# Optimization experiments

Measured on AMD Instinct MI355X. Metric: run time of the kernel, lower is better.

Reference implementation:

```python
import jax, jax.numpy as jnp
import numpy as np

DIM = 96; NH = 3; HD = DIM // NH; SCALE = HD ** -0.5
WS = (7, 7, 7); N = WS[0] * WS[1] * WS[2]
SHIFT = (3, 3, 3)  # half window
NL = 2
GRID = (28, 28, 28)
B = 2


def _rel_index():
    wd, wh, ww = WS
    coords = np.stack(np.meshgrid(np.arange(wd), np.arange(wh), np.arange(ww), indexing='ij')).reshape(3, -1)
    rel = (coords[:, :, None] - coords[:, None, :]).transpose(1, 2, 0)  # [N,N,3]
    rel[..., 0] += wd - 1; rel[..., 1] += wh - 1; rel[..., 2] += ww - 1
    rel[..., 0] *= (2 * wh - 1) * (2 * ww - 1); rel[..., 1] *= (2 * ww - 1)
    return rel.sum(-1)  # [N,N]

REL_IDX = _rel_index()


def _window_partition(x):
    b, D, H, W, C = x.shape
    wd, wh, ww = WS
    x = x.reshape(b, D // wd, wd, H // wh, wh, W // ww, ww, C)
    x = x.transpose(0, 1, 3, 5, 2, 4, 6, 7)
    return x.reshape(-1, N, C)


def _window_reverse(win, b, D, H, W):
    wd, wh, ww = WS
    C = win.shape[-1]
    x = win.reshape(b, D // wd, H // wh, W // ww, wd, wh, ww, C)
    x = x.transpose(0, 1, 4, 2, 5, 3, 6, 7)
    return x.reshape(b, D, H, W, C)


def _compute_mask():
    # MONAI compute_mask for the shifted (SW-MSA) block
    D, H, W = GRID; wd, wh, ww = WS; sd, sh, sw = SHIFT
    img = np.zeros((1, D, H, W, 1), np.float32)
    cnt = 0
    for d in (slice(-wd), slice(-wd, -sd), slice(-sd, None)):
        for h in (slice(-wh), slice(-wh, -sh), slice(-sh, None)):
            for w in (slice(-ww), slice(-ww, -sw), slice(-sw, None)):
                img[:, d, h, w, :] = cnt; cnt += 1
    mw = img.reshape(1, D // wd, wd, H // wh, wh, W // ww, ww, 1)
    mw = mw.transpose(0, 1, 3, 5, 2, 4, 6, 7).reshape(-1, N)  # [nw, N]
    am = mw[:, None, :] - mw[:, :, None]
    return np.where(am != 0, np.float32(-100.0), np.float32(0.0))

MASK = jnp.asarray(_compute_mask())  # [nw, N, N]


def _ln(x, g, b):
    mu = x.mean(-1, keepdims=True)
    var = ((x - mu) ** 2).mean(-1, keepdims=True)
    return (x - mu) / jnp.sqrt(var + 1e-5) * g + b


def _block(x, p, shift, mask):
    b, D, H, W, C = x.shape
    h = _ln(x, p['n1g'], p['n1b'])
    if shift is not None:
        h = jnp.roll(h, (-shift[0], -shift[1], -shift[2]), axis=(1, 2, 3))
    xw = _window_partition(h)  # [b*nw, N, C]
    Bn = xw.shape[0]
    qkv = (xw @ p['qkvw'].T + p['qkvb']).reshape(Bn, N, 3, NH, HD).transpose(2, 0, 3, 1, 4)
    q, k, v = qkv[0] * SCALE, qkv[1], qkv[2]
    attn = jnp.einsum('bhnd,bhmd->bhnm', q, k)
    bias = p['rel'][REL_IDX.reshape(-1)].reshape(N, N, NH).transpose(2, 0, 1)
    attn = attn + bias[None]
    if mask is not None:
        nw = mask.shape[0]
        attn = (attn.reshape(Bn // nw, nw, NH, N, N) + mask[None, :, None]).reshape(Bn, NH, N, N)
    attn = jax.nn.softmax(attn, axis=-1)
    out = jnp.einsum('bhnm,bhmd->bhnd', attn, v).transpose(0, 2, 1, 3).reshape(Bn, N, C)
    out = out @ p['projw'].T + p['projb']
    h = _window_reverse(out, b, D, H, W)
    if shift is not None:
        h = jnp.roll(h, shift, axis=(1, 2, 3))
    x = x + h
    m = _ln(x, p['n2g'], p['n2b'])
    m = jax.nn.gelu(m @ p['fc1w'].T + p['fc1b'], approximate=False) @ p['fc2w'].T + p['fc2b']
    return x + m


def setup_inputs() -> dict:
    key = jax.random.key(0)
    ks = jax.random.split(key, 8)
    nbias = (2 * WS[0] - 1) * (2 * WS[1] - 1) * (2 * WS[2] - 1)
    return {
        'x': jax.random.normal(ks[0], (B,) + GRID + (DIM,), jnp.float32),
        'norm1_g': jnp.ones((NL, DIM), jnp.float32),
        'norm1_b': jnp.zeros((NL, DIM), jnp.float32),
        'qkv_w': jax.random.normal(ks[1], (NL, 3 * DIM, DIM), jnp.float32) * 0.02,
        'qkv_b': jnp.zeros((NL, 3 * DIM), jnp.float32),
        'rel_bias': jax.random.normal(ks[2], (NL, nbias, NH), jnp.float32) * 0.02,
        'proj_w': jax.random.normal(ks[3], (NL, DIM, DIM), jnp.float32) * 0.02,
        'proj_b': jnp.zeros((NL, DIM), jnp.float32),
        'norm2_g': jnp.ones((NL, DIM), jnp.float32),
        'norm2_b': jnp.zeros((NL, DIM), jnp.float32),
        'fc1_w': jax.random.normal(ks[4], (NL, 4 * DIM, DIM), jnp.float32) * 0.02,
        'fc1_b': jnp.zeros((NL, 4 * DIM), jnp.float32),
        'fc2_w': jax.random.normal(ks[5], (NL, DIM, 4 * DIM), jnp.float32) * 0.02,
        'fc2_b': jnp.zeros((NL, DIM), jnp.float32),
    }


def reference(x, norm1_g, norm1_b, qkv_w, qkv_b, rel_bias, proj_w, proj_b,
              norm2_g, norm2_b, fc1_w, fc1_b, fc2_w, fc2_b):
    for i in range(NL):
        p = dict(n1g=norm1_g[i], n1b=norm1_b[i], qkvw=qkv_w[i], qkvb=qkv_b[i],
                 rel=rel_bias[i], projw=proj_w[i], projb=proj_b[i],
                 n2g=norm2_g[i], n2b=norm2_b[i], fc1w=fc1_w[i], fc1b=fc1_b[i],
                 fc2w=fc2_w[i], fc2b=fc2_b[i])
        if i % 2 == 0:
            x = _block(x, p, None, None)  # W-MSA (mask is all-zero for shift=0)
        else:
            x = _block(x, p, SHIFT, MASK)  # SW-MSA
    return x
```

## Files before the change

kernel.cpp:

```cpp
#include <hip/hip_runtime.h>
#include <math.h>

#define DIM 96
#define NHD 3
#define HD 32
#define NWT 343
#define NWIN 128
#define TOK 43904
#define NBIAS 2197
#define SCALE 0.17677669529663687f
#define TPAD 352
#define QTS 5632
#define HSZ (22 * QTS)

typedef __attribute__((ext_vector_type(8))) short bf16x8;
typedef __attribute__((ext_vector_type(4))) float f32x4;

__device__ __forceinline__ unsigned short f2b(float f) {
    union { float f; unsigned int u; } x; x.f = f;
    unsigned int r = (x.u + 0x7fffu + ((x.u >> 16) & 1u)) >> 16;
    return (unsigned short)r;
}
__device__ __forceinline__ unsigned int pk2bf(float a, float b) {
    union { float f; unsigned int u; } x, y; x.f = a; y.f = b;
    return ((x.u + 0x8000u) >> 16) | ((y.u + 0x8000u) & 0xffff0000u);
}
__device__ __forceinline__ float lo16(unsigned int u) {
    union { unsigned int u; float f; } x; x.u = u << 16; return x.f;
}
__device__ __forceinline__ float hi16(unsigned int u) {
    union { unsigned int u; float f; } x; x.u = u & 0xffff0000u; return x.f;
}

__global__ void __launch_bounds__(256) k_cvt4(
        const float* __restrict__ s0, const float* __restrict__ s1,
        const float* __restrict__ s2, const float* __restrict__ s3,
        unsigned short* __restrict__ dst) {
    int i = blockIdx.x * 256 + threadIdx.x;
    if (i >= 221184) return;
    const float* src; int off;
    if (i < 55296)       { src = s0; off = i; }
    else if (i < 73728)  { src = s1; off = i - 55296; }
    else if (i < 147456) { src = s2; off = i - 73728; }
    else                 { src = s3; off = i - 147456; }
    dst[i] = f2b(src[off]);
}

__global__ void __launch_bounds__(256) k_bias(
        const float* __restrict__ rel0, const float* __restrict__ rel1,
        unsigned short* __restrict__ bt) {
    int i = blockIdx.x * 256 + threadIdx.x;
    if (i >= 27 * HSZ) return;
    int off = i % QTS;
    int t = i / QTS;
    int qt = t % 22; t /= 22;
    int head = t % 3; int combo = t / 3;
    int j = off & 7, q4i = (off >> 3) & 3, lm = (off >> 5) & 15, pr = off >> 9;
    int q = min(qt * 16 + lm, 342);
    int kcol = pr * 32 + ((j >> 2) << 4) + q4i * 4 + (j & 3);
    float outv;
    if (kcol >= 343) {
        outv = -100000.0f;
    } else {
        int dq = q / 49, hq = (q / 7) % 7, wq = q % 7;
        int dk = kcol / 49, hk = (kcol / 7) % 7, wk = kcol % 7;
        int ridx = (dq - dk + 6) * 169 + (hq - hk + 6) * 13 + (wq - wk + 6);
        const float* rel = (combo == 0) ? rel0 : rel1;
        float b = rel[ridx * 3 + head];
        if (combo > 0) {
            int ty = combo - 1;
            int rqd = (ty & 4) ? 1 + (dq >= 4) : 0;
            int rqh = (ty & 2) ? 1 + (hq >= 4) : 0;
            int rqw = (ty & 1) ? 1 + (wq >= 4) : 0;
            int rkd = (ty & 4) ? 1 + (dk >= 4) : 0;
            int rkh = (ty & 2) ? 1 + (hk >= 4) : 0;
            int rkw = (ty & 1) ? 1 + (wk >= 4) : 0;
            if (rqd != rkd || rqh != rkh || rqw != rkw) b -= 100.0f;
        }
        outv = b;
    }
    bt[i] = f2b(outv);
}

__global__ void __launch_bounds__(256) k_qkv(
        const float* __restrict__ x, const float* __restrict__ g1,
        const float* __restrict__ b1, const unsigned short* __restrict__ W,
        const float* __restrict__ bias, unsigned short* __restrict__ q,
        unsigned short* __restrict__ k, unsigned short* __restrict__ v, int shift) {
    __shared__ __align__(16) unsigned short lns[64][104];
    __shared__ __align__(16) unsigned short wbuf[96][104];
    int wid = threadIdx.x >> 6, lane = threadIdx.x & 63;
    int lm = lane & 15, q4 = lane >> 4;
    int m0 = blockIdx.x * 64 + wid * 16;
    int bwr[4], nnr[4];
    size_t rowoff[4];
    #pragma unroll
    for (int r = 0; r < 4; ++r) {
        int wtok = m0 + q4 * 4 + r;
        int bw = wtok / NWT, n = wtok % NWT;
        bwr[r] = bw; nnr[r] = n;
        int b = bw >> 6, win = bw & 63;
        int wdi = win >> 4, whi = (win >> 2) & 3, wwi = win & 3;
        int d = n / 49, h = (n / 7) % 7, w = n % 7;
        int sd = (wdi * 7 + d + shift) % 28;
        int sh = (whi * 7 + h + shift) % 28;
        int sw = (wwi * 7 + w + shift) % 28;
        rowoff[r] = (((size_t)(b * 28 + sd) * 28 + sh) * 28 + sw) * 96;
    }
    float val[6][4], g1v[6], b1v[6];
    #pragma unroll
    for (int c = 0; c < 6; ++c) {
        int ncol = c * 16 + lm;
        g1v[c] = g1[ncol]; b1v[c] = b1[ncol];
        #pragma unroll
        for (int r = 0; r < 4; ++r) val[c][r] = x[rowoff[r] + ncol];
    }
    #pragma unroll
    for (int r = 0; r < 4; ++r) {
        float s = 0.f, s2 = 0.f;
        #pragma unroll
        for (int c = 0; c < 6; ++c) { s += val[c][r]; s2 += val[c][r] * val[c][r]; }
        #pragma unroll
        for (int off = 8; off > 0; off >>= 1) {
            s  += __shfl_xor(s,  off, 64);
            s2 += __shfl_xor(s2, off, 64);
        }
        float mu = s * (1.0f / 96.0f);
        float rstd = rsqrtf(s2 * (1.0f / 96.0f) - mu * mu + 1e-5f);
        int row = wid * 16 + q4 * 4 + r;
        #pragma unroll
        for (int c = 0; c < 6; ++c)
            lns[row][c * 16 + lm] = f2b((val[c][r] - mu) * rstd * g1v[c] + b1v[c]);
    }
    __syncthreads();
    bf16x8 a1[3];
    #pragma unroll
    for (int ks = 0; ks < 3; ++ks)
        a1[ks] = *((const bf16x8*)&lns[wid * 16 + lm][ks * 32 + q4 * 8]);
    for (int ch = 0; ch < 3; ++ch) {
        __syncthreads();
        const uint4* src = (const uint4*)(W + ch * 96 * 96);
        for (int s = threadIdx.x; s < 1152; s += 256) {
            int row = s / 12, seg = s % 12;
            *((uint4*)&wbuf[row][seg * 8]) = src[s];
        }
        __syncthreads();
        f32x4 acc[6];
        #pragma unroll
        for (int c = 0; c < 6; ++c) acc[c] = (f32x4){0.f, 0.f, 0.f, 0.f};
        #pragma unroll
        for (int ks = 0; ks < 3; ++ks) {
            #pragma unroll
            for (int c = 0; c < 6; ++c) {
                bf16x8 b = *((const bf16x8*)&wbuf[c * 16 + lm][ks * 32 + q4 * 8]);
                acc[c] = __builtin_amdgcn_mfma_f32_16x16x32_bf16(a1[ks], b, acc[c], 0, 0, 0);
            }
        }
        #pragma unroll
        for (int c = 0; c < 6; ++c) {
            int col = c * 16 + lm;
            int head = col >> 5, hd = col & 31;
            float bb = bias[ch * 96 + col];
            #pragma unroll
            for (int r = 0; r < 4; ++r) {
                int wh = bwr[r] * NHD + head;
                float vv = acc[c][r] + bb;
                if (ch == 0)
                    q[(size_t)wh * (TPAD * 32) + nnr[r] * 32 + hd] = f2b(vv * SCALE);
                else if (ch == 1)
                    k[(size_t)wh * (TPAD * 32) + nnr[r] * 32 + hd] = f2b(vv);
                else
                    v[(size_t)wh * (32 * TPAD) + hd * TPAD + nnr[r]] = f2b(vv);
            }
        }
    }
}

__global__ void __launch_bounds__(256) k_attn(
        const unsigned short* __restrict__ q, const unsigned short* __restrict__ k,
        const unsigned short* __restrict__ vT, const unsigned short* __restrict__ bt,
        unsigned short* __restrict__ o, int tmul) {
    __shared__ __align__(16) unsigned short vts[32 * 360];
    __shared__ __align__(16) unsigned short pbuf[4][2][16 * 40];
    int wh = blockIdx.x / 3, third = blockIdx.x % 3;
    int bw = wh / NHD, head = wh % NHD;
    const unsigned int* vsrc = (const unsigned int*)(vT + (size_t)wh * 32 * TPAD);
    unsigned int* vdst = (unsigned int*)vts;
    for (int i = threadIdx.x; i < 32 * 176; i += 256) {
        int row = i / 176, cc = i - row * 176;
        vdst[row * 180 + cc] = vsrc[i];
    }
    __syncthreads();
    int win = bw & 63;
    int wdi = win >> 4, whi = (win >> 2) & 3, wwi = win & 3;
    int type = ((wdi == 3) ? 4 : 0) | ((whi == 3) ? 2 : 0) | ((wwi == 3) ? 1 : 0);
    const unsigned short* bbase = bt + (size_t)type * tmul + (size_t)head * HSZ;
    int wid = threadIdx.x >> 6, lane = threadIdx.x & 63;
    int lm = lane & 15, q4 = lane >> 4;
    int tb = third * 8 + wid * 2;
    if (tb > 21) return;
    bool dual = (tb + 1 <= 21);
    int qtA = tb, qtB = dual ? tb + 1 : tb;
    const unsigned short* qbase = q + (size_t)wh * TPAD * 32;
    const unsigned short* kbase = k + (size_t)wh * TPAD * 32;
    int qtokA = qtA * 16 + lm, qtokB = qtB * 16 + lm;
    bf16x8 qfA = *((const bf16x8*)(qbase + qtokA * 32 + q4 * 8));
    bf16x8 qfB = *((const bf16x8*)(qbase + qtokB * 32 + q4 * 8));
    const unsigned short* bpA = bbase + (size_t)qtA * QTS + lm * 32 + q4 * 8;
    const unsigned short* bpB = bbase + (size_t)qtB * QTS + lm * 32 + q4 * 8;
    f32x4 aA0 = (f32x4){0.f,0.f,0.f,0.f}, aA1 = aA0, aB0 = aA0, aB1 = aA0;
    float dA = 0.f, dB = 0.f;
    unsigned short* pbA = pbuf[wid][0];
    unsigned short* pbB = pbuf[wid][1];
    bf16x8 kf0n = *((const bf16x8*)(kbase + lm * 32 + q4 * 8));
    bf16x8 kf1n = *((const bf16x8*)(kbase + (16 + lm) * 32 + q4 * 8));
    uint4 bAn = *((const uint4*)bpA);
    uint4 bBn = *((const uint4*)bpB);
    for (int pr = 0; pr < 11; ++pr) {
        int kb0 = pr * 32;
        bf16x8 kf0 = kf0n, kf1 = kf1n;
        uint4 uA = bAn, uB = bBn;
        if (pr < 10) {
            int kb1 = kb0 + 32;
            kf0n = *((const bf16x8*)(kbase + (kb1 + lm) * 32 + q4 * 8));
            kf1n = *((const bf16x8*)(kbase + (kb1 + 16 + lm) * 32 + q4 * 8));
            bAn = *((const uint4*)(bpA + (pr + 1) * 512));
            bBn = *((const uint4*)(bpB + (pr + 1) * 512));
        }
        f32x4 z = (f32x4){0.f, 0.f, 0.f, 0.f};
        f32x4 sA0 = __builtin_amdgcn_mfma_f32_16x16x32_bf16(kf0, qfA, z, 0, 0, 0);
        f32x4 sA1 = __builtin_amdgcn_mfma_f32_16x16x32_bf16(kf1, qfA, z, 0, 0, 0);
        f32x4 sB0 = __builtin_amdgcn_mfma_f32_16x16x32_bf16(kf0, qfB, z, 0, 0, 0);
        f32x4 sB1 = __builtin_amdgcn_mfma_f32_16x16x32_bf16(kf1, qfB, z, 0, 0, 0);
        float pA[8], pB[8];
        pA[0] = __expf(sA0[0] + lo16(uA.x)); pA[1] = __expf(sA0[1] + hi16(uA.x));
        pA[2] = __expf(sA0[2] + lo16(uA.y)); pA[3] = __expf(sA0[3] + hi16(uA.y));
        pA[4] = __expf(sA1[0] + lo16(uA.z)); pA[5] = __expf(sA1[1] + hi16(uA.z));
        pA[6] = __expf(sA1[2] + lo16(uA.w)); pA[7] = __expf(sA1[3] + hi16(uA.w));
        pB[0] = __expf(sB0[0] + lo16(uB.x)); pB[1] = __expf(sB0[1] + hi16(uB.x));
        pB[2] = __expf(sB0[2] + lo16(uB.y)); pB[3] = __expf(sB0[3] + hi16(uB.y));
        pB[4] = __expf(sB1[0] + lo16(uB.z)); pB[5] = __expf(sB1[1] + hi16(uB.z));
        pB[6] = __expf(sB1[2] + lo16(uB.w)); pB[7] = __expf(sB1[3] + hi16(uB.w));
        #pragma unroll
        for (int j = 0; j < 8; ++j) { dA += pA[j]; dB += pB[j]; }
        #pragma unroll
        for (int t = 0; t < 2; ++t) {
            *((unsigned int*)(pbA + lm * 40 + t * 16 + q4 * 4)) =
                pk2bf(pA[t * 4 + 0], pA[t * 4 + 1]);
            *((unsigned int*)(pbA + lm * 40 + t * 16 + q4 * 4 + 2)) =
                pk2bf(pA[t * 4 + 2], pA[t * 4 + 3]);
            *((unsigned int*)(pbB + lm * 40 + t * 16 + q4 * 4)) =
                pk2bf(pB[t * 4 + 0], pB[t * 4 + 1]);
            *((unsigned int*)(pbB + lm * 40 + t * 16 + q4 * 4 + 2)) =
                pk2bf(pB[t * 4 + 2], pB[t * 4 + 3]);
        }
        bf16x8 pfA = *((const bf16x8*)(pbA + lm * 40 + q4 * 8));
        bf16x8 pfB = *((const bf16x8*)(pbB + lm * 40 + q4 * 8));
        bf16x8 v0 = *((const bf16x8*)(vts + lm * 360 + kb0 + q4 * 8));
        bf16x8 v1 = *((const bf16x8*)(vts + (16 + lm) * 360 + kb0 + q4 * 8));
        aA0 = __builtin_amdgcn_mfma_f32_16x16x32_bf16(pfA, v0, aA0, 0, 0, 0);
        aA1 = __builtin_amdgcn_mfma_f32_16x16x32_bf16(pfA, v1, aA1, 0, 0, 0);
        aB0 = __builtin_amdgcn_mfma_f32_16x16x32_bf16(pfB, v0, aB0, 0, 0, 0);
        aB1 = __builtin_amdgcn_mfma_f32_16x16x32_bf16(pfB, v1, aB1, 0, 0, 0);
    }
    dA += __shfl_xor(dA, 16, 64); dA += __shfl_xor(dA, 32, 64);
    dB += __shfl_xor(dB, 16, 64); dB += __shfl_xor(dB, 32, 64);
    #pragma unroll
    for (int r = 0; r < 4; ++r) {
        int qrowA = qtA * 16 + q4 * 4 + r;
        if (qrowA < NWT) {
            float inv = 1.0f / __shfl(dA, q4 * 4 + r, 64);
            unsigned short* op = o + (size_t)(bw * NWT + qrowA) * DIM + head * HD;
            op[lm]      = f2b(aA0[r] * inv);
            op[16 + lm] = f2b(aA1[r] * inv);
        }
    }
    if (dual) {
        #pragma unroll
        for (int r = 0; r < 4; ++r) {
            int qrowB = qtB * 16 + q4 * 4 + r;
            if (qrowB < NWT) {
                float inv = 1.0f / __shfl(dB, q4 * 4 + r, 64);
                unsigned short* op = o + (size_t)(bw * NWT + qrowB) * DIM + head * HD;
                op[lm]      = f2b(aB0[r] * inv);
                op[16 + lm] = f2b(aB1[r] * inv);
            }
        }
    }
}

__global__ void __launch_bounds__(256) k_pm(
        const unsigned short* __restrict__ ao, const unsigned short* __restrict__ Wp,
        const float* __restrict__ pbias, const float* __restrict__ xin,
        float* __restrict__ xout,
        const float* __restrict__ g2, const float* __restrict__ b2,
        const unsigned short* __restrict__ w1, const float* __restrict__ bb1,
        const unsigned short* __restrict__ w2, const float* __restrict__ bb2,
        int shift) {
    __shared__ __align__(16) unsigned short lns[64][104];
    __shared__ __align__(16) unsigned short big[18816];
    int wid = threadIdx.x >> 6, lane = threadIdx.x & 63;
    int lm = lane & 15, q4 = lane >> 4;
    int m0 = blockIdx.x * 64 + wid * 16;
    for (int s = threadIdx.x; s < 1152; s += 256) {
        int row = s / 12, seg = s % 12;
        *((uint4*)&big[row * 104 + seg * 8]) = ((const uint4*)Wp)[s];
    }
    const unsigned short* arow = ao + (size_t)(m0 + lm) * 96;
    bf16x8 a1[3];
    #pragma unroll
    for (int ks = 0; ks < 3; ++ks)
        a1[ks] = *((const bf16x8*)(arow + ks * 32 + q4 * 8));
    __syncthreads();
    f32x4 acc[6];
    #pragma unroll
    for (int c = 0; c < 6; ++c) acc[c] = (f32x4){0.f, 0.f, 0.f, 0.f};
    #pragma unroll
    for (int ks = 0; ks < 3; ++ks) {
        #pragma unroll
        for (int c = 0; c < 6; ++c) {
            bf16x8 b = *((const bf16x8*)&big[(c * 16 + lm) * 104 + ks * 32 + q4 * 8]);
            acc[c] = __builtin_amdgcn_mfma_f32_16x16x32_bf16(a1[ks], b, acc[c], 0, 0, 0);
        }
    }
    size_t rowoff[4];
    #pragma unroll
    for (int r = 0; r < 4; ++r) {
        int wtok = m0 + q4 * 4 + r;
        int bw = wtok / NWT, n = wtok % NWT;
        int b = bw >> 6, win = bw & 63;
        int wdi = win >> 4, whi = (win >> 2) & 3, wwi = win & 3;
        int d = n / 49, h = (n / 7) % 7, w = n % 7;
        int sd = (wdi * 7 + d + shift) % 28;
        int sh = (whi * 7 + h + shift) % 28;
        int sw = (wwi * 7 + w + shift) % 28;
        rowoff[r] = (((size_t)(b * 28 + sd) * 28 + sh) * 28 + sw) * 96;
    }
    float val[6][4], g2v[6], b2v[6];
    #pragma unroll
    for (int c = 0; c < 6; ++c) {
        int n = c * 16 + lm;
        float bb = pbias[n];
        g2v[c] = g2[n]; b2v[c] = b2[n];
        #pragma unroll
        for (int r = 0; r < 4; ++r)
            val[c][r] = xin[rowoff[r] + n] + acc[c][r] + bb;
    }
    #pragma unroll
    for (int r = 0; r < 4; ++r) {
        float s = 0.f, s2 = 0.f;
        #pragma unroll
        for (int c = 0; c < 6; ++c) { s += val[c][r]; s2 += val[c][r] * val[c][r]; }
        #pragma unroll
        for (int off = 8; off > 0; off >>= 1) {
            s  += __shfl_xor(s,  off, 64);
            s2 += __shfl_xor(s2, off, 64);
        }
        float mu = s * (1.0f / 96.0f);
        float rstd = rsqrtf(s2 * (1.0f / 96.0f) - mu * mu + 1e-5f);
        int row = wid * 16 + q4 * 4 + r;
        #pragma unroll
        for (int c = 0; c < 6; ++c)
            lns[row][c * 16 + lm] = f2b((val[c][r] - mu) * rstd * g2v[c] + b2v[c]);
    }
    bf16x8 am[3];
    #pragma unroll
    for (int ks = 0; ks < 3; ++ks)
        am[ks] = *((const bf16x8*)&lns[wid * 16 + lm][ks * 32 + q4 * 8]);
    f32x4 acc2[6];
    #pragma unroll
    for (int c = 0; c < 6; ++c) acc2[c] = (f32x4){0.f, 0.f, 0.f, 0.f};
    unsigned short* hid_ = &big[13952 + wid * 1216];
    for (int ch = 0; ch < 6; ++ch) {
        __syncthreads();
        const uint4* src1 = (const uint4*)(w1 + ch * 64 * 96);
        #pragma unroll
        for (int t = 0; t < 3; ++t) {
            int s = threadIdx.x + t * 256;
            int row = s / 12, seg = s % 12;
            *((uint4*)&big[row * 104 + seg * 8]) = src1[s];
        }
        #pragma unroll
        for (int t = 0; t < 3; ++t) {
            int s = threadIdx.x + t * 256;
            int row = s >> 3, seg = s & 7;
            *((uint4*)&big[6656 + row * 76 + seg * 8]) =
                *((const uint4*)(w2 + row * 384 + ch * 64 + seg * 8));
        }
        __syncthreads();
        f32x4 acc1[4];
        #pragma unroll
        for (int t = 0; t < 4; ++t) acc1[t] = (f32x4){0.f, 0.f, 0.f, 0.f};
        #pragma unroll
        for (int ks = 0; ks < 3; ++ks) {
            #pragma unroll
            for (int t = 0; t < 4; ++t) {
                bf16x8 b = *((const bf16x8*)&big[(t * 16 + lm) * 104 + ks * 32 + q4 * 8]);
                acc1[t] = __builtin_amdgcn_mfma_f32_16x16x32_bf16(am[ks], b, acc1[t], 0, 0, 0);
            }
        }
        #pragma unroll
        for (int t = 0; t < 4; ++t) {
            float bb = bb1[ch * 64 + t * 16 + lm];
            #pragma unroll
            for (int r = 0; r < 4; ++r) {
                float v2 = acc1[t][r] + bb;
                float t2 = v2 * v2;
                float m = fmaf(-0.0713548162f, t2, -1.5957691216f);
                float e = __expf(v2 * m);
                float ge = v2 * (1.0f / (1.0f + e));
                hid_[(q4 * 4 + r) * 76 + t * 16 + lm] = f2b(ge);
            }
        }
        #pragma unroll
        for (int ks2 = 0; ks2 < 2; ++ks2) {
            bf16x8 a = *((const bf16x8*)(hid_ + lm * 76 + ks2 * 32 + q4 * 8));
            #pragma unroll
            for (int c = 0; c < 6; ++c) {
                bf16x8 b = *((const bf16x8*)&big[6656 + (c * 16 + lm) * 76 + ks2 * 32 + q4 * 8]);
                acc2[c] = __builtin_amdgcn_mfma_f32_16x16x32_bf16(a, b, acc2[c], 0, 0, 0);
            }
        }
    }
    #pragma unroll
    for (int c = 0; c < 6; ++c) {
        int n = c * 16 + lm;
        float bb = bb2[n];
        #pragma unroll
        for (int r = 0; r < 4; ++r)
            xout[rowoff[r] + n] = val[c][r] + acc2[c][r] + bb;
    }
}

extern "C" void kernel_launch(void* const* d_in, const int* in_sizes, int n_in,
                              void* d_out, int out_size, void* d_ws, size_t ws_size,
                              hipStream_t stream) {
    const float* x     = (const float*)d_in[0];
    const float* n1g   = (const float*)d_in[1];
    const float* n1b   = (const float*)d_in[2];
    const float* qkvw  = (const float*)d_in[3];
    const float* qkvb  = (const float*)d_in[4];
    const float* relb  = (const float*)d_in[5];
    const float* projw = (const float*)d_in[6];
    const float* projb = (const float*)d_in[7];
    const float* n2g   = (const float*)d_in[8];
    const float* n2b   = (const float*)d_in[9];
    const float* fc1w  = (const float*)d_in[10];
    const float* fc1b  = (const float*)d_in[11];
    const float* fc2w  = (const float*)d_in[12];
    const float* fc2b  = (const float*)d_in[13];
    float* out = (float*)d_out;

    const size_t NEL = (size_t)TOK * DIM;
    const size_t QKN = (size_t)NWIN * NHD * TPAD * 32;
    float* buf_x = (float*)d_ws;
    unsigned short* hbuf = (unsigned short*)(buf_x + NEL);
    unsigned short* bq   = hbuf + NEL;
    unsigned short* bk   = bq + QKN;
    unsigned short* bv   = bk + QKN;
    unsigned short* wts  = bv + QKN;
    unsigned short* wq  = wts;
    unsigned short* wp  = wq + 2 * 27648;
    unsigned short* w1  = wp + 2 * 9216;
    unsigned short* w2  = w1 + 2 * 36864;
    unsigned short* btab = wts + 221184;

    k_cvt4<<<(221184 + 255) / 256, 256, 0, stream>>>(qkvw, projw, fc1w, fc2w, wts);
    k_bias<<<(27 * HSZ + 255) / 256, 256, 0, stream>>>(
        relb, relb + NBIAS * NHD, btab);

    for (int L = 0; L < 2; ++L) {
        int shift = (L == 0) ? 0 : 3;
        const float* xin_l = (L == 0) ? x : buf_x;
        float* xfin = (L == 0) ? buf_x : out;
        const unsigned short* btL = (L == 0) ? btab : btab + 3 * HSZ;
        int tmul = (L == 0) ? 0 : 3 * HSZ;

        k_qkv<<<TOK / 64, 256, 0, stream>>>(xin_l, n1g + L * 96, n1b + L * 96,
                                            wq + L * 27648, qkvb + L * 288,
                                            bq, bk, bv, shift);
        k_attn<<<NWIN * NHD * 3, 256, 0, stream>>>(bq, bk, bv, btL, hbuf, tmul);
        k_pm<<<TOK / 64, 256, 0, stream>>>(hbuf, wp + L * 9216, projb + L * 96,
                                           xin_l, xfin,
                                           n2g + L * 96, n2b + L * 96,
                                           w1 + L * 36864, fc1b + L * 384,
                                           w2 + L * 36864, fc2b + L * 96, shift);
    }
}
```

Baseline: 266.4 us.

## Fuse all stages into one persistent cooperative kernel with grid syncs

Replaces the eight separate launches (weight conversion, bias table, and per-layer qkv/attention/MLP) with a single persistent cooperative kernel. It loops over virtual blocks per stage and separates stages with grid.sync(). This removes per-launch overhead and launch gaps, at the cost of grid-wide barriers, a grid capped at 768 resident blocks, and shared memory sized for the largest stage, which may reduce occupancy for the qkv and attention stages. A fallback path keeps the multi-kernel launch if the cooperative launch fails.

```diff
diff --git a/kernel.cpp b/kernel.cpp
--- a/kernel.cpp
+++ b/kernel.cpp
@@ -1,5 +1,8 @@
 #include <hip/hip_runtime.h>
+#include <hip/hip_cooperative_groups.h>
 #include <math.h>
+
+namespace cg = cooperative_groups;
 
 #define DIM 96
 #define NHD 3
@@ -12,6 +15,8 @@
 #define TPAD 352
 #define QTS 5632
 #define HSZ (22 * QTS)
+#define NQKV 686
+#define NATT 1152
 
 typedef __attribute__((ext_vector_type(8))) short bf16x8;
 typedef __attribute__((ext_vector_type(4))) float f32x4;
@@ -32,25 +37,18 @@
     union { unsigned int u; float f; } x; x.u = u & 0xffff0000u; return x.f;
 }
 
-__global__ void __launch_bounds__(256) k_cvt4(
-        const float* __restrict__ s0, const float* __restrict__ s1,
-        const float* __restrict__ s2, const float* __restrict__ s3,
-        unsigned short* __restrict__ dst) {
-    int i = blockIdx.x * 256 + threadIdx.x;
-    if (i >= 221184) return;
+__device__ __forceinline__ unsigned short cvt_elem(
+        int i, const float* s0, const float* s1, const float* s2, const float* s3) {
     const float* src; int off;
     if (i < 55296)       { src = s0; off = i; }
     else if (i < 73728)  { src = s1; off = i - 55296; }
     else if (i < 147456) { src = s2; off = i - 73728; }
     else                 { src = s3; off = i - 147456; }
-    dst[i] = f2b(src[off]);
-}
-
-__global__ void __launch_bounds__(256) k_bias(
-        const float* __restrict__ rel0, const float* __restrict__ rel1,
-        unsigned short* __restrict__ bt) {
-    int i = blockIdx.x * 256 + threadIdx.x;
-    if (i >= 27 * HSZ) return;
+    return f2b(src[off]);
+}
+
+__device__ __forceinline__ unsigned short bias_elem(
+        int i, const float* rel0, const float* rel1) {
     int off = i % QTS;
     int t = i / QTS;
     int qt = t % 22; t /= 22;
@@ -79,19 +77,20 @@
         }
         outv = b;
     }
-    bt[i] = f2b(outv);
-}
-
-__global__ void __launch_bounds__(256) k_qkv(
-        const float* __restrict__ x, const float* __restrict__ g1,
+    return f2b(outv);
+}
+
+__device__ __forceinline__ void qkv_block(
+        int vb, const float* __restrict__ x, const float* __restrict__ g1,
         const float* __restrict__ b1, const unsigned short* __restrict__ W,
         const float* __restrict__ bias, unsigned short* __restrict__ q,
-        unsigned short* __restrict__ k, unsigned short* __restrict__ v, int shift) {
-    __shared__ __align__(16) unsigned short lns[64][104];
-    __shared__ __align__(16) unsigned short wbuf[96][104];
+        unsigned short* __restrict__ k, unsigned short* __restrict__ v,
+        int shift, unsigned short* sm) {
+    unsigned short* lns = sm;
+    unsigned short* wbuf = sm + 6656;
     int wid = threadIdx.x >> 6, lane = threadIdx.x & 63;
     int lm = lane & 15, q4 = lane >> 4;
-    int m0 = blockIdx.x * 64 + wid * 16;
+    int m0 = vb * 64 + wid * 16;
     int bwr[4], nnr[4];
     size_t rowoff[4];
     #pragma unroll
@@ -130,19 +129,19 @@
         int row = wid * 16 + q4 * 4 + r;
         #pragma unroll
         for (int c = 0; c < 6; ++c)
-            lns[row][c * 16 + lm] = f2b((val[c][r] - mu) * rstd * g1v[c] + b1v[c]);
+            lns[row * 104 + c * 16 + lm] = f2b((val[c][r] - mu) * rstd * g1v[c] + b1v[c]);
     }
     __syncthreads();
     bf16x8 a1[3];
     #pragma unroll
     for (int ks = 0; ks < 3; ++ks)
-        a1[ks] = *((const bf16x8*)&lns[wid * 16 + lm][ks * 32 + q4 * 8]);
+        a1[ks] = *((const bf16x8*)(lns + (wid * 16 + lm) * 104 + ks * 32 + q4 * 8));
     for (int ch = 0; ch < 3; ++ch) {
         __syncthreads();
         const uint4* src = (const uint4*)(W + ch * 96 * 96);
         for (int s = threadIdx.x; s < 1152; s += 256) {
             int row = s / 12, seg = s % 12;
-            *((uint4*)&wbuf[row][seg * 8]) = src[s];
+            *((uint4*)(wbuf + row * 104 + seg * 8)) = src[s];
         }
         __syncthreads();
         f32x4 acc[6];
@@ -152,7 +151,7 @@
         for (int ks = 0; ks < 3; ++ks) {
             #pragma unroll
             for (int c = 0; c < 6; ++c) {
-                bf16x8 b = *((const bf16x8*)&wbuf[c * 16 + lm][ks * 32 + q4 * 8]);
+                bf16x8 b = *((const bf16x8*)(wbuf + (c * 16 + lm) * 104 + ks * 32 + q4 * 8));
                 acc[c] = __builtin_amdgcn_mfma_f32_16x16x32_bf16(a1[ks], b, acc[c], 0, 0, 0);
             }
         }
@@ -176,14 +175,15 @@
     }
 }
 
-__global__ void __launch_bounds__(256) k_attn(
-        const unsigned short* __restrict__ q, const unsigned short* __restrict__ k,
+__device__ __forceinline__ void attn_block(
+        int vb, const unsigned short* __restrict__ q, const unsigned short* __restrict__ k,
         const unsigned short* __restrict__ vT, const unsigned short* __restrict__ bt,
-        unsigned short* __restrict__ o, int tmul) {
-    __shared__ __align__(16) unsigned short vts[32 * 360];
-    __shared__ __align__(16) unsigned short pbuf[4][2][16 * 40];
-    int wh = blockIdx.x / 3, third = blockIdx.x % 3;
+        unsigned short* __restrict__ o, int tmul, unsigned short* sm) {
+    unsigned short* vts = sm;
+    unsigned short* pbase = sm + 11520;
+    int wh = vb / 3, third = vb % 3;
     int bw = wh / NHD, head = wh % NHD;
+    __syncthreads();
     const unsigned int* vsrc = (const unsigned int*)(vT + (size_t)wh * 32 * TPAD);
     unsigned int* vdst = (unsigned int*)vts;
     for (int i = threadIdx.x; i < 32 * 176; i += 256) {
@@ -210,8 +210,8 @@
     const unsigned short* bpB = bbase + (size_t)qtB * QTS + lm * 32 + q4 * 8;
     f32x4 aA0 = (f32x4){0.f,0.f,0.f,0.f}, aA1 = aA0, aB0 = aA0, aB1 = aA0;
     float dA = 0.f, dB = 0.f;
-    unsigned short* pbA = pbuf[wid][0];
-    unsigned short* pbB = pbuf[wid][1];
+    unsigned short* pbA = pbase + wid * 1280;
+    unsigned short* pbB = pbA + 640;
     bf16x8 kf0n = *((const bf16x8*)(kbase + lm * 32 + q4 * 8));
     bf16x8 kf1n = *((const bf16x8*)(kbase + (16 + lm) * 32 + q4 * 8));
     uint4 bAn = *((const uint4*)bpA);
@@ -289,22 +289,23 @@
     }
 }
 
-__global__ void __launch_bounds__(256) k_pm(
-        const unsigned short* __restrict__ ao, const unsigned short* __restrict__ Wp,
+__device__ __forceinline__ void pm_block(
+        int vb, const unsigned short* __restrict__ ao, const unsigned short* __restrict__ Wp,
         const float* __restrict__ pbias, const float* __restrict__ xin,
         float* __restrict__ xout,
         const float* __restrict__ g2, const float* __restrict__ b2,
         const unsigned short* __restrict__ w1, const float* __restrict__ bb1,
         const unsigned short* __restrict__ w2, const float* __restrict__ bb2,
-        int shift) {
-    __shared__ __align__(16) unsigned short lns[64][104];
-    __shared__ __align__(16) unsigned short big[18816];
+        int shift, unsigned short* sm) {
+    unsigned short* lns = sm;
+    unsigned short* big = sm + 6656;
     int wid = threadIdx.x >> 6, lane = threadIdx.x & 63;
     int lm = lane & 15, q4 = lane >> 4;
-    int m0 = blockIdx.x * 64 + wid * 16;
+    int m0 = vb * 64 + wid * 16;
+    __syncthreads();
     for (int s = threadIdx.x; s < 1152; s += 256) {
         int row = s / 12, seg = s % 12;
-        *((uint4*)&big[row * 104 + seg * 8]) = ((const uint4*)Wp)[s];
+        *((uint4*)(big + row * 104 + seg * 8)) = ((const uint4*)Wp)[s];
     }
     const unsigned short* arow = ao + (size_t)(m0 + lm) * 96;
     bf16x8 a1[3];
@@ -319,7 +320,7 @@
     for (int ks = 0; ks < 3; ++ks) {
         #pragma unroll
         for (int c = 0; c < 6; ++c) {
-            bf16x8 b = *((const bf16x8*)&big[(c * 16 + lm) * 104 + ks * 32 + q4 * 8]);
+            bf16x8 b = *((const bf16x8*)(big + (c * 16 + lm) * 104 + ks * 32 + q4 * 8));
             acc[c] = __builtin_amdgcn_mfma_f32_16x16x32_bf16(a1[ks], b, acc[c], 0, 0, 0);
         }
     }
@@ -361,16 +362,16 @@
         int row = wid * 16 + q4 * 4 + r;
         #pragma unroll
         for (int c = 0; c < 6; ++c)
-            lns[row][c * 16 + lm] = f2b((val[c][r] - mu) * rstd * g2v[c] + b2v[c]);
+            lns[row * 104 + c * 16 + lm] = f2b((val[c][r] - mu) * rstd * g2v[c] + b2v[c]);
     }
     bf16x8 am[3];
     #pragma unroll
     for (int ks = 0; ks < 3; ++ks)
-        am[ks] = *((const bf16x8*)&lns[wid * 16 + lm][ks * 32 + q4 * 8]);
+        am[ks] = *((const bf16x8*)(lns + (wid * 16 + lm) * 104 + ks * 32 + q4 * 8));
     f32x4 acc2[6];
     #pragma unroll
     for (int c = 0; c < 6; ++c) acc2[c] = (f32x4){0.f, 0.f, 0.f, 0.f};
-    unsigned short* hid_ = &big[13952 + wid * 1216];
+    unsigned short* hid_ = big + 13952 + wid * 1216;
     for (int ch = 0; ch < 6; ++ch) {
         __syncthreads();
         const uint4* src1 = (const uint4*)(w1 + ch * 64 * 96);
@@ -378,13 +379,13 @@
         for (int t = 0; t < 3; ++t) {
             int s = threadIdx.x + t * 256;
             int row = s / 12, seg = s % 12;
-            *((uint4*)&big[row * 104 + seg * 8]) = src1[s];
+            *((uint4*)(big + row * 104 + seg * 8)) = src1[s];
         }
         #pragma unroll
         for (int t = 0; t < 3; ++t) {
             int s = threadIdx.x + t * 256;
             int row = s >> 3, seg = s & 7;
-            *((uint4*)&big[6656 + row * 76 + seg * 8]) =
+            *((uint4*)(big + 6656 + row * 76 + seg * 8)) =
                 *((const uint4*)(w2 + row * 384 + ch * 64 + seg * 8));
         }
         __syncthreads();
@@ -395,7 +396,7 @@
         for (int ks = 0; ks < 3; ++ks) {
             #pragma unroll
             for (int t = 0; t < 4; ++t) {
-                bf16x8 b = *((const bf16x8*)&big[(t * 16 + lm) * 104 + ks * 32 + q4 * 8]);
+                bf16x8 b = *((const bf16x8*)(big + (t * 16 + lm) * 104 + ks * 32 + q4 * 8));
                 acc1[t] = __builtin_amdgcn_mfma_f32_16x16x32_bf16(am[ks], b, acc1[t], 0, 0, 0);
             }
         }
@@ -417,7 +418,7 @@
             bf16x8 a = *((const bf16x8*)(hid_ + lm * 76 + ks2 * 32 + q4 * 8));
             #pragma unroll
             for (int c = 0; c < 6; ++c) {
-                bf16x8 b = *((const bf16x8*)&big[6656 + (c * 16 + lm) * 76 + ks2 * 32 + q4 * 8]);
+                bf16x8 b = *((const bf16x8*)(big + 6656 + (c * 16 + lm) * 76 + ks2 * 32 + q4 * 8));
                 acc2[c] = __builtin_amdgcn_mfma_f32_16x16x32_bf16(a, b, acc2[c], 0, 0, 0);
             }
         }
@@ -430,6 +431,81 @@
         for (int r = 0; r < 4; ++r)
             xout[rowoff[r] + n] = val[c][r] + acc2[c][r] + bb;
     }
+}
+
+struct KP {
+    const float *x, *n1g, *n1b, *qkvw, *qkvb, *relb, *projw, *projb;
+    const float *n2g, *n2b, *fc1w, *fc1b, *fc2w, *fc2b;
+    float *out, *buf_x;
+    unsigned short *hbuf, *bq, *bk, *bv, *wts, *btab;
+};
+
+__global__ void __launch_bounds__(256, 3) k_all(KP p) {
+    __shared__ __align__(16) unsigned short sm[25472];
+    cg::grid_group grid = cg::this_grid();
+    int nb = gridDim.x;
+    for (int i = blockIdx.x * 256 + threadIdx.x; i < 221184; i += nb * 256)
+        p.wts[i] = cvt_elem(i, p.qkvw, p.projw, p.fc1w, p.fc2w);
+    const float* rel1 = p.relb + NBIAS * NHD;
+    for (int i = blockIdx.x * 256 + threadIdx.x; i < 27 * HSZ; i += nb * 256)
+        p.btab[i] = bias_elem(i, p.relb, rel1);
+    grid.sync();
+    unsigned short* wq = p.wts;
+    unsigned short* wp = wq + 2 * 27648;
+    unsigned short* w1 = wp + 2 * 9216;
+    unsigned short* w2 = w1 + 2 * 36864;
+    for (int L = 0; L < 2; ++L) {
+        int shift = (L == 0) ? 0 : 3;
+        const float* xin = (L == 0) ? p.x : p.buf_x;
+        float* xfin = (L == 0) ? p.buf_x : p.out;
+        const unsigned short* btL = (L == 0) ? p.btab : p.btab + 3 * HSZ;
+        int tmul = (L == 0) ? 0 : 3 * HSZ;
+        for (int vb = blockIdx.x; vb < NQKV; vb += nb)
+            qkv_block(vb, xin, p.n1g + L * 96, p.n1b + L * 96, wq + L * 27648,
+                      p.qkvb + L * 288, p.bq, p.bk, p.bv, shift, sm);
+        grid.sync();
+        for (int vb = blockIdx.x; vb < NATT; vb += nb)
+            attn_block(vb, p.bq, p.bk, p.bv, btL, p.hbuf, tmul, sm);
+        grid.sync();
+        for (int vb = blockIdx.x; vb < NQKV; vb += nb)
+            pm_block(vb, p.hbuf, wp + L * 9216, p.projb + L * 96, xin, xfin,
+                     p.n2g + L * 96, p.n2b + L * 96, w1 + L * 36864, p.fc1b + L * 384,
+                     w2 + L * 36864, p.fc2b + L * 96, shift, sm);
+        if (L == 0) grid.sync();
+    }
+}
+
+__global__ void __launch_bounds__(256) k_cvt4(
+        const float* s0, const float* s1, const float* s2, const float* s3,
+        unsigned short* dst) {
+    int i = blockIdx.x * 256 + threadIdx.x;
+    if (i < 221184) dst[i] = cvt_elem(i, s0, s1, s2, s3);
+}
+__global__ void __launch_bounds__(256) k_bias(
+        const float* rel0, const float* rel1, unsigned short* bt) {
+    int i = blockIdx.x * 256 + threadIdx.x;
+    if (i < 27 * HSZ) bt[i] = bias_elem(i, rel0, rel1);
+}
+__global__ void __launch_bounds__(256) k_qkv_w(
+        const float* x, const float* g1, const float* b1, const unsigned short* W,
+        const float* bias, unsigned short* q, unsigned short* k, unsigned short* v,
+        int shift) {
+    __shared__ __align__(16) unsigned short sm[16640];
+    qkv_block(blockIdx.x, x, g1, b1, W, bias, q, k, v, shift, sm);
+}
+__global__ void __launch_bounds__(256) k_attn_w(
+        const unsigned short* q, const unsigned short* k, const unsigned short* vT,
+        const unsigned short* bt, unsigned short* o, int tmul) {
+    __shared__ __align__(16) unsigned short sm[16640];
+    attn_block(blockIdx.x, q, k, vT, bt, o, tmul, sm);
+}
+__global__ void __launch_bounds__(256) k_pm_w(
+        const unsigned short* ao, const unsigned short* Wp, const float* pbias,
+        const float* xin, float* xout, const float* g2, const float* b2,
+        const unsigned short* w1, const float* bb1,
+        const unsigned short* w2, const float* bb2, int shift) {
+    __shared__ __align__(16) unsigned short sm[25472];
+    pm_block(blockIdx.x, ao, Wp, pbias, xin, xout, g2, b2, w1, bb1, w2, bb2, shift, sm);
 }
 
 extern "C" void kernel_launch(void* const* d_in, const int* in_sizes, int n_in,
@@ -459,31 +535,44 @@
     unsigned short* bk   = bq + QKN;
     unsigned short* bv   = bk + QKN;
     unsigned short* wts  = bv + QKN;
-    unsigned short* wq  = wts;
-    unsigned short* wp  = wq + 2 * 27648;
-    unsigned short* w1  = wp + 2 * 9216;
-    unsigned short* w2  = w1 + 2 * 36864;
     unsigned short* btab = wts + 221184;
 
-    k_cvt4<<<(221184 + 255) / 256, 256, 0, stream>>>(qkvw, projw, fc1w, fc2w, wts);
-    k_bias<<<(27 * HSZ + 255) / 256, 256, 0, stream>>>(
-        relb, relb + NBIAS * NHD, btab);
-
-    for (int L = 0; L < 2; ++L) {
-        int shift = (L == 0) ? 0 : 3;
-        const float* xin_l = (L == 0) ? x : buf_x;
-        float* xfin = (L == 0) ? buf_x : out;
-        const unsigned short* btL = (L == 0) ? btab : btab + 3 * HSZ;
-        int tmul = (L == 0) ? 0 : 3 * HSZ;
-
-        k_qkv<<<TOK / 64, 256, 0, stream>>>(xin_l, n1g + L * 96, n1b + L * 96,
-                                            wq + L * 27648, qkvb + L * 288,
-                                            bq, bk, bv, shift);
-        k_attn<<<NWIN * NHD * 3, 256, 0, stream>>>(bq, bk, bv, btL, hbuf, tmul);
-        k_pm<<<TOK / 64, 256, 0, stream>>>(hbuf, wp + L * 9216, projb + L * 96,
-                                           xin_l, xfin,
-                                           n2g + L * 96, n2b + L * 96,
-                                           w1 + L * 36864, fc1b + L * 384,
-                                           w2 + L * 36864, fc2b + L * 96, shift);
-    }
-}
+    KP p;
+    p.x = x; p.n1g = n1g; p.n1b = n1b; p.qkvw = qkvw; p.qkvb = qkvb; p.relb = relb;
+    p.projw = projw; p.projb = projb; p.n2g = n2g; p.n2b = n2b;
+    p.fc1w = fc1w; p.fc1b = fc1b; p.fc2w = fc2w; p.fc2b = fc2b;
+    p.out = out; p.buf_x = buf_x;
+    p.hbuf = hbuf; p.bq = bq; p.bk = bk; p.bv = bv; p.wts = wts; p.btab = btab;
+
+    int maxBlk = 0;
+    hipError_t qerr = hipOccupancyMaxActiveBlocksPerMultiprocessor(&maxBlk, k_all, 256, 0);
+    if (qerr != hipSuccess || maxBlk < 1) maxBlk = 1;
+    int grid = maxBlk * 256;
+    if (grid > 768) grid = 768;
+    void* args[] = { &p };
+    hipError_t err = hipLaunchCooperativeKernel((const void*)k_all, dim3(grid), dim3(256),
+                                                args, 0, stream);
+    if (err != hipSuccess) {
+        k_cvt4<<<(221184 + 255) / 256, 256, 0, stream>>>(qkvw, projw, fc1w, fc2w, wts);
+        k_bias<<<(27 * HSZ + 255) / 256, 256, 0, stream>>>(relb, relb + NBIAS * NHD, btab);
+        unsigned short* wq = wts;
+        unsigned short* wp = wq + 2 * 27648;
+        unsigned short* w1 = wp + 2 * 9216;
+        unsigned short* w2 = w1 + 2 * 36864;
+        for (int L = 0; L < 2; ++L) {
+            int shift = (L == 0) ? 0 : 3;
+            const float* xin_l = (L == 0) ? x : buf_x;
+            float* xfin = (L == 0) ? buf_x : out;
+            const unsigned short* btL = (L == 0) ? btab : btab + 3 * HSZ;
+            int tmul = (L == 0) ? 0 : 3 * HSZ;
+            k_qkv_w<<<NQKV, 256, 0, stream>>>(xin_l, n1g + L * 96, n1b + L * 96,
+                                              wq + L * 27648, qkvb + L * 288,
+                                              bq, bk, bv, shift);
+            k_attn_w<<<NATT, 256, 0, stream>>>(bq, bk, bv, btL, hbuf, tmul);
+            k_pm_w<<<NQKV, 256, 0, stream>>>(hbuf, wp + L * 9216, projb + L * 96,
+                                             xin_l, xfin, n2g + L * 96, n2b + L * 96,
+                                             w1 + L * 36864, fc1b + L * 384,
+                                             w2 + L * 36864, fc2b + L * 96, shift);
+        }
+    }
+}
```

Result: slower. 721.0 us (+170.7%).
